# Kernel tuning notes

Hardware: AMD Instinct MI355X
Metric: run time of the kernel (lower is better)

Reference implementation:

```python
import jax, jax.numpy as jnp
import numpy as np

N_ATOMS = 32768
DEG = 16            # directed neighbors per atom
N_RBF = 6
CUTOFF = 5.0
ENV_P = 6


def _build_graph():
    # circular-offset neighbor structure so every (j,i) / (k,j) pair in
    # angle_list exists exactly once in nbr_list (required by m_idx_of_angles)
    half = DEG // 2
    offs = np.concatenate([np.arange(1, half + 1), N_ATOMS - np.arange(1, half + 1)])  # [DEG]
    j = np.arange(N_ATOMS)
    nbr_dst = (j[:, None] + offs[None, :]) % N_ATOMS                    # [N, DEG]
    nbr_list = np.stack([np.repeat(j, DEG), nbr_dst.reshape(-1)], 1)    # [E, 2]
    o1, o2 = np.meshgrid(offs, offs, indexing='ij')
    keep = o1 != o2
    o1, o2 = o1[keep], o2[keep]                                         # [DEG*(DEG-1)]
    i = (j[:, None] + o1[None, :]) % N_ATOMS
    k = (j[:, None] + o2[None, :]) % N_ATOMS
    jc = np.broadcast_to(j[:, None], i.shape)
    angle_list = np.stack([i.reshape(-1), jc.reshape(-1), k.reshape(-1)], 1)  # [T, 3]
    return nbr_list.astype(np.int64), angle_list.astype(np.int64)


def setup_inputs() -> dict:
    key = jax.random.key(0)
    nbr, ang = _build_graph()
    xyz = jax.random.normal(key, (N_ATOMS, 3), dtype=jnp.float32) * 3.0
    return {"xyz": xyz, "nbr_list": jnp.asarray(nbr), "angle_list": jnp.asarray(ang)}


def _match_edge(nbr_list, src, dst):
    # efficient, mathematically identical replacement for the O(T*E)
    # broadcast-mask + nonzero() in m_idx_of_angles (each edge is unique)
    keys = nbr_list[:, 0] * N_ATOMS + nbr_list[:, 1]
    order = jnp.argsort(keys)
    pos = jnp.searchsorted(keys[order], src * N_ATOMS + dst)
    return order[pos]


def _envelope(x):
    p = ENV_P
    a = -(p + 1) * (p + 2) / 2.0
    b = float(p * (p + 2))
    c = -p * (p + 1) / 2.0
    return 1.0 / x + a * x ** (p - 1) + b * x ** p + c * x ** (p + 1)


def reference(xyz, nbr_list, angle_list):
    # --- edge distances ---
    diff = xyz[nbr_list[:, 0]] - xyz[nbr_list[:, 1]]          # [E, 3]
    d = jnp.linalg.norm(diff, axis=-1)                        # [E]
    # --- triplet angles (compute_angle) ---
    r_ji = xyz[angle_list[:, 0]] - xyz[angle_list[:, 1]]      # [T, 3]
    r_jk = xyz[angle_list[:, 2]] - xyz[angle_list[:, 1]]      # [T, 3]
    dot = jnp.sum(r_ji * r_jk, axis=-1)
    crs = jnp.linalg.norm(jnp.cross(r_ji, r_jk), axis=-1)
    alpha = jnp.arctan2(crs, dot)                             # [T]
    # --- radial basis with polynomial envelope ---
    n = jnp.arange(1, N_RBF + 1, dtype=xyz.dtype)
    dc = (d / CUTOFF)[:, None]                                # [E, 1]
    e_rbf = _envelope(dc) * jnp.sin(n * jnp.pi * dc)          # [E, N_RBF]
    # --- triplet->edge index matching (m_idx_of_angles) ---
    ji_idx = _match_edge(nbr_list, angle_list[:, 1], angle_list[:, 0])  # [T]
    kj_idx = _match_edge(nbr_list, angle_list[:, 2], angle_list[:, 1])  # [T]
    # --- gather-compute-scatter stage (interaction-block aggregation) ---
    trip = alpha[:, None] * e_rbf[kj_idx]                     # [T, N_RBF]
    out = jax.ops.segment_sum(trip, ji_idx, num_segments=nbr_list.shape[0])  # [E, N_RBF]
    return out
```

## Files before the change

### kernel.cpp

```cpp
#include <hip/hip_runtime.h>
#include <math.h>


constexpr int N_ATOMS = 32768;
constexpr int DEG = 16;
constexpr int N_RBF = 6;
constexpr int ATOMS_PER_BLOCK = 16;
constexpr float CUTOFF = 5.0f;

__global__ __launch_bounds__(256) void dimenet_fused(const float* __restrict__ xyz,
                                                     float* __restrict__ out) {
    const int tid = threadIdx.x;
    const int a   = tid >> 4;
    const int m   = tid & 15;
    const int j   = blockIdx.x * ATOMS_PER_BLOCK + a;

    __shared__ float s_rel[ATOMS_PER_BLOCK][DEG][3];
    __shared__ float s_rbf[ATOMS_PER_BLOCK][DEG][N_RBF];

    const int off = (m < 8) ? (m + 1) : (7 - m);
    const int nbr = (j + off + N_ATOMS) & (N_ATOMS - 1);

    const float jx = xyz[3 * j + 0], jy = xyz[3 * j + 1], jz = xyz[3 * j + 2];
    const float rx = xyz[3 * nbr + 0] - jx;
    const float ry = xyz[3 * nbr + 1] - jy;
    const float rz = xyz[3 * nbr + 2] - jz;
    s_rel[a][m][0] = rx;
    s_rel[a][m][1] = ry;
    s_rel[a][m][2] = rz;

    const float d  = sqrtf(rx * rx + ry * ry + rz * rz);
    const float x  = d * (1.0f / CUTOFF);
    const float x2  = x * x;
    const float x5  = x2 * x2 * x;
    const float env = 1.0f / x + x5 * (-28.0f + x * (48.0f - 21.0f * x));

    float s1, c1;
    sincosf((float)M_PI * x, &s1, &c1);
    float sn = s1, cn = c1;
    s_rbf[a][m][0] = env * s1;
#pragma unroll
    for (int n = 1; n < N_RBF; ++n) {
        const float sn1 = sn * c1 + cn * s1;
        const float cn1 = cn * c1 - sn * s1;
        sn = sn1;
        cn = cn1;
        s_rbf[a][m][n] = env * sn;
    }

    __syncthreads();

    const float ax = rx, ay = ry, az = rz;
    float acc[N_RBF] = {0.f, 0.f, 0.f, 0.f, 0.f, 0.f};
#pragma unroll
    for (int t = 1; t < DEG; ++t) {
        const int m2 = (m + t) & 15;
        const float bx = s_rel[a][m2][0];
        const float by = s_rel[a][m2][1];
        const float bz = s_rel[a][m2][2];
        const float dot = ax * bx + ay * by + az * bz;
        const float cx = ay * bz - az * by;
        const float cy = az * bx - ax * bz;
        const float cz = ax * by - ay * bx;
        const float crs   = sqrtf(cx * cx + cy * cy + cz * cz);
        const float alpha = atan2f(crs, dot);
#pragma unroll
        for (int n = 0; n < N_RBF; ++n)
            acc[n] += alpha * s_rbf[a][m2][n];
    }

    float* o = out + (size_t)(j * DEG + m) * N_RBF;
#pragma unroll
    for (int n = 0; n < N_RBF; ++n) o[n] = acc[n];
}

extern "C" void kernel_launch(void* const* d_in, const int* in_sizes, int n_in,
                              void* d_out, int out_size, void* d_ws, size_t ws_size,
                              hipStream_t stream) {
    const float* xyz = (const float*)d_in[0];
    float* out = (float*)d_out;
    dim3 grid(N_ATOMS / ATOMS_PER_BLOCK);
    dim3 block(256);
    hipLaunchKernelGGL(dimenet_fused, grid, block, 0, stream, xyz, out);
}
```

Measured before the change: 141.0 us.

## Replace atan2 of cross norm with half-angle polynomial; vectorize shared memory

Computes the triplet angle from the dot product and the product of edge lengths through a half-angle identity, atan2(|a×b|, a·b) = 2·atan(sqrt((|a||b|-a·b)/(|a||b|+a·b))). The atan is evaluated with a short minimax polynomial plus a reflection, which removes the cross product, a sqrt and the library atan2f from the inner loop. Edge vectors and lengths are packed as float4, and the RBF values as two float4 per edge, so shared-memory traffic uses wide loads. Output stores become float2, and fast rcp/sqrt intrinsics are used. The polynomial atan and the approximate intrinsics lose some accuracy, and the sqrt/rcp form may lose precision when the two edges are nearly collinear.

```diff
diff --git a/kernel.cpp b/kernel.cpp
--- a/kernel.cpp
+++ b/kernel.cpp
@@ -5,7 +5,7 @@
 constexpr int N_ATOMS = 32768;
 constexpr int DEG = 16;
 constexpr int N_RBF = 6;
-constexpr int ATOMS_PER_BLOCK = 16;
+constexpr int APB = 16;
 constexpr float CUTOFF = 5.0f;
 
 __global__ __launch_bounds__(256) void dimenet_fused(const float* __restrict__ xyz,
@@ -13,10 +13,10 @@
     const int tid = threadIdx.x;
     const int a   = tid >> 4;
     const int m   = tid & 15;
-    const int j   = blockIdx.x * ATOMS_PER_BLOCK + a;
+    const int j   = blockIdx.x * APB + a;
 
-    __shared__ float s_rel[ATOMS_PER_BLOCK][DEG][3];
-    __shared__ float s_rbf[ATOMS_PER_BLOCK][DEG][N_RBF];
+    __shared__ float4 s_rel[APB][DEG];
+    __shared__ float4 s_rbf[APB][DEG][2];
 
     const int off = (m < 8) ? (m + 1) : (7 - m);
     const int nbr = (j + off + N_ATOMS) & (N_ATOMS - 1);
@@ -25,53 +25,76 @@
     const float rx = xyz[3 * nbr + 0] - jx;
     const float ry = xyz[3 * nbr + 1] - jy;
     const float rz = xyz[3 * nbr + 2] - jz;
-    s_rel[a][m][0] = rx;
-    s_rel[a][m][1] = ry;
-    s_rel[a][m][2] = rz;
+    const float d  = __builtin_amdgcn_sqrtf(rx * rx + ry * ry + rz * rz);
+    s_rel[a][m] = make_float4(rx, ry, rz, d);
 
-    const float d  = sqrtf(rx * rx + ry * ry + rz * rz);
     const float x  = d * (1.0f / CUTOFF);
-    const float x2  = x * x;
-    const float x5  = x2 * x2 * x;
-    const float env = 1.0f / x + x5 * (-28.0f + x * (48.0f - 21.0f * x));
+    const float x2 = x * x, x5 = x2 * x2 * x;
+    const float env = __builtin_amdgcn_rcpf(x) + x5 * (-28.0f + x * (48.0f - 21.0f * x));
 
     float s1, c1;
     sincosf((float)M_PI * x, &s1, &c1);
     float sn = s1, cn = c1;
-    s_rbf[a][m][0] = env * s1;
-#pragma unroll
-    for (int n = 1; n < N_RBF; ++n) {
-        const float sn1 = sn * c1 + cn * s1;
-        const float cn1 = cn * c1 - sn * s1;
-        sn = sn1;
-        cn = cn1;
-        s_rbf[a][m][n] = env * sn;
+    float r0 = env * s1, r1, r2, r3, r4, r5;
+    {
+        float t;
+        t = sn * c1 + cn * s1; cn = cn * c1 - sn * s1; sn = t; r1 = env * sn;
+        t = sn * c1 + cn * s1; cn = cn * c1 - sn * s1; sn = t; r2 = env * sn;
+        t = sn * c1 + cn * s1; cn = cn * c1 - sn * s1; sn = t; r3 = env * sn;
+        t = sn * c1 + cn * s1; cn = cn * c1 - sn * s1; sn = t; r4 = env * sn;
+        t = sn * c1 + cn * s1; cn = cn * c1 - sn * s1; sn = t; r5 = env * sn;
     }
+    s_rbf[a][m][0] = make_float4(r0, r1, r2, r3);
+    s_rbf[a][m][1] = make_float4(r4, r5, 0.f, 0.f);
 
     __syncthreads();
 
-    const float ax = rx, ay = ry, az = rz;
-    float acc[N_RBF] = {0.f, 0.f, 0.f, 0.f, 0.f, 0.f};
+    const float C0 =  2.0f * 0.99997726f;
+    const float C1 = -2.0f * 0.33262347f;
+    const float C2 =  2.0f * 0.19354346f;
+    const float C3 = -2.0f * 0.11643287f;
+    const float C4 =  2.0f * 0.05265332f;
+    const float C5 = -2.0f * 0.01172120f;
+    const float PI_F = 3.14159265358979f;
+
+    float acc0 = 0.f, acc1 = 0.f, acc2 = 0.f, acc3 = 0.f, acc4 = 0.f, acc5 = 0.f;
+
 #pragma unroll
     for (int t = 1; t < DEG; ++t) {
         const int m2 = (m + t) & 15;
-        const float bx = s_rel[a][m2][0];
-        const float by = s_rel[a][m2][1];
-        const float bz = s_rel[a][m2][2];
-        const float dot = ax * bx + ay * by + az * bz;
-        const float cx = ay * bz - az * by;
-        const float cy = az * bx - ax * bz;
-        const float cz = ax * by - ay * bx;
-        const float crs   = sqrtf(cx * cx + cy * cy + cz * cz);
-        const float alpha = atan2f(crs, dot);
-#pragma unroll
-        for (int n = 0; n < N_RBF; ++n)
-            acc[n] += alpha * s_rbf[a][m2][n];
+        const float4 rr = s_rel[a][m2];
+        const float dot = rx * rr.x + ry * rr.y + rz * rr.z;
+        const float u   = d * rr.w;
+        const float num = u - dot;
+        const float den = u + dot;
+        float mn = fminf(num, den);
+        float mx = fmaxf(num, den);
+        mn = fmaxf(mn, 0.0f);
+        mx = fmaxf(mx, 1e-30f);
+        const float z  = __builtin_amdgcn_sqrtf(mn * __builtin_amdgcn_rcpf(mx));
+        const float zs = z * z;
+        float p = fmaf(zs, C5, C4);
+        p = fmaf(zs, p, C3);
+        p = fmaf(zs, p, C2);
+        p = fmaf(zs, p, C1);
+        p = fmaf(zs, p, C0);
+        const float at2   = z * p;
+        const float alpha = (num <= den) ? at2 : (PI_F - at2);
+
+        const float4 b0 = s_rbf[a][m2][0];
+        const float4 b1 = s_rbf[a][m2][1];
+        acc0 = fmaf(alpha, b0.x, acc0);
+        acc1 = fmaf(alpha, b0.y, acc1);
+        acc2 = fmaf(alpha, b0.z, acc2);
+        acc3 = fmaf(alpha, b0.w, acc3);
+        acc4 = fmaf(alpha, b1.x, acc4);
+        acc5 = fmaf(alpha, b1.y, acc5);
     }
 
-    float* o = out + (size_t)(j * DEG + m) * N_RBF;
-#pragma unroll
-    for (int n = 0; n < N_RBF; ++n) o[n] = acc[n];
+    float2* o = (float2*)(out + (size_t)(j * DEG + m) * N_RBF);
+    o[0] = make_float2(acc0, acc1);
+    o[1] = make_float2(acc2, acc3);
+    o[2] = make_float2(acc4, acc5);
 }
 
 extern "C" void kernel_launch(void* const* d_in, const int* in_sizes, int n_in,
@@ -79,7 +102,7 @@
                               hipStream_t stream) {
     const float* xyz = (const float*)d_in[0];
     float* out = (float*)d_out;
-    dim3 grid(N_ATOMS / ATOMS_PER_BLOCK);
+    dim3 grid(N_ATOMS / APB);
     dim3 block(256);
     hipLaunchKernelGGL(dimenet_fused, grid, block, 0, stream, xyz, out);
 }
```

Result: faster. 132.2 us (-6.2%).
